# Optimization experiments

Measured on AMD Instinct MI355X. Metric: run time of the kernel, lower is better.

Reference implementation:

```python
import jax, jax.numpy as jnp
import numpy as np

N = 100000
E = 1600000
D_IN = 128
D_H = 128
D_OUT = 128
K = 2
EPS = 0.1


def setup_inputs() -> dict:
    key = jax.random.key(0)
    ks = jax.random.split(key, 10)
    x = jax.random.normal(ks[0], (N, D_IN), dtype=jnp.float32)
    edge_index = jax.random.randint(ks[1], (2, E), 0, N, dtype=jnp.int64)
    # parameters (scaled like torch default inits, small uniform)
    def lin(k, fan_in, shape):
        bound = 1.0 / np.sqrt(fan_in)
        return jax.random.uniform(k, shape, jnp.float32, -bound, bound)
    emb_w = lin(ks[2], D_IN, (D_IN, D_H))
    emb_b = lin(ks[3], D_IN, (D_H,))
    # TAGConv: K+1 linears (no bias) + one output bias
    conv_ws = jnp.stack([lin(ks[4 + i], D_H, (D_H, D_H)) for i in range(K + 1)])
    conv_b = lin(ks[7], D_H, (D_H,))
    ro_w = lin(ks[8], D_H, (D_H, D_OUT))
    ro_b = lin(ks[9], D_H, (D_OUT,))
    return {
        "x": x, "edge_index": edge_index, "delta_t": 4,
        "emb_w": emb_w, "emb_b": emb_b,
        "conv_ws": conv_ws, "conv_b": conv_b,
        "ro_w": ro_w, "ro_b": ro_b,
    }


def _tagconv(h, src, dst, norm, conv_ws, conv_b):
    """PyG TAGConv: out = sum_k W_k (A_hat^k h) + b, A_hat = D^-1/2 A D^-1/2 (no self loops)."""
    out = h @ conv_ws[0]
    xk = h
    for k in range(1, K + 1):
        msg = norm[:, None] * xk[src]            # [E, D_H] gather
        xk = jax.ops.segment_sum(msg, dst, num_segments=h.shape[0])  # scatter-add
        out = out + xk @ conv_ws[k]
    return out + conv_b


def reference(x, edge_index, delta_t, emb_w, emb_b, conv_ws, conv_b, ro_w, ro_b):
    src = edge_index[0]
    dst = edge_index[1]
    n = x.shape[0]
    # gcn_norm without self loops: deg over targets of unit edge weights
    deg = jnp.zeros((n,), jnp.float32).at[dst].add(1.0)
    dinv = jnp.where(deg > 0, jax.lax.rsqrt(jnp.maximum(deg, 1.0)), 0.0)
    norm = dinv[src] * dinv[dst]                 # [E]

    h = x @ emb_w + emb_b
    h_middle = h
    for _ in range(int(delta_t)):
        conv = _tagconv(h, src, dst, norm, conv_ws, conv_b)
        h_middle = h + 0.5 * EPS * jnp.tanh(conv)
        conv_mid = _tagconv(h_middle, src, dst, norm, conv_ws, conv_b)
        h = h + EPS * jnp.tanh(conv_mid)
    y = h_middle @ ro_w + ro_b
    return (y, h_middle)
```

## Files before the change

### kernel.cpp

```cpp
#include <hip/hip_runtime.h>
#include <hip/hip_bf16.h>

#define NN 100000
#define EE 1600000
#define DD 128
#define EPSc 0.1f

typedef unsigned short bfu;
typedef __attribute__((ext_vector_type(8))) short short8;
typedef __attribute__((ext_vector_type(4))) float f32x4;
typedef __attribute__((ext_vector_type(2))) float f32x2;

__device__ __forceinline__ float bf2f(bfu s) {
    union { unsigned u; float f; } c; c.u = ((unsigned)s) << 16; return c.f;
}
__device__ __forceinline__ bfu f2bf(float f) {
    union { float f; unsigned u; } c; c.f = f;
    unsigned u = c.u + 0x7fffu + ((c.u >> 16) & 1u);
    return (bfu)(u >> 16);
}
__device__ __forceinline__ unsigned pk8(float a, float b, float c, float d) {
    int r = 0;
    r = __builtin_amdgcn_cvt_pk_fp8_f32(a, b, r, false);
    r = __builtin_amdgcn_cvt_pk_fp8_f32(c, d, r, true);
    return (unsigned)r;
}
__device__ __forceinline__ unsigned char enc8(float a) {
    return (unsigned char)(__builtin_amdgcn_cvt_pk_fp8_f32(a, a, 0, false) & 0xFF);
}
__device__ __forceinline__ short8 e8bf(uint2 u) {
    f32x2 p0 = __builtin_amdgcn_cvt_pk_f32_fp8((int)u.x, false);
    f32x2 p1 = __builtin_amdgcn_cvt_pk_f32_fp8((int)u.x, true);
    f32x2 p2 = __builtin_amdgcn_cvt_pk_f32_fp8((int)u.y, false);
    f32x2 p3 = __builtin_amdgcn_cvt_pk_f32_fp8((int)u.y, true);
    short8 s;
    s[0] = (short)f2bf(p0[0]); s[1] = (short)f2bf(p0[1]);
    s[2] = (short)f2bf(p1[0]); s[3] = (short)f2bf(p1[1]);
    s[4] = (short)f2bf(p2[0]); s[5] = (short)f2bf(p2[1]);
    s[6] = (short)f2bf(p3[0]); s[7] = (short)f2bf(p3[1]);
    return s;
}


__global__ __launch_bounds__(256) void count_deg_kernel(const int* __restrict__ dst,
                                                        int* __restrict__ ideg, int e_cnt) {
    int e = blockIdx.x * 256 + threadIdx.x;
    if (e < e_cnt) atomicAdd(&ideg[dst[e]], 1);
}

__global__ __launch_bounds__(256) void dinv_kernel(const int* __restrict__ ideg,
                                                   float* __restrict__ dinv, int n) {
    int i = blockIdx.x * 256 + threadIdx.x;
    if (i < n) {
        int d = ideg[i];
        dinv[i] = (d > 0) ? rsqrtf((float)d) : 0.0f;
    }
}

__global__ __launch_bounds__(256) void partial_sum_kernel(const int* __restrict__ ideg,
                                                          int* __restrict__ partials, int n) {
    __shared__ int sm[256];
    int i = blockIdx.x * 256 + threadIdx.x;
    sm[threadIdx.x] = (i < n) ? ideg[i] : 0;
    __syncthreads();
    for (int off = 128; off > 0; off >>= 1) {
        if ((int)threadIdx.x < off) sm[threadIdx.x] += sm[threadIdx.x + off];
        __syncthreads();
    }
    if (threadIdx.x == 0) partials[blockIdx.x] = sm[0];
}

__global__ __launch_bounds__(512) void scan_partials_kernel(int* __restrict__ partials,
                                                            int* __restrict__ row_ptr,
                                                            int nb, int n) {
    __shared__ int sm[512];
    int v = ((int)threadIdx.x < nb) ? partials[threadIdx.x] : 0;
    sm[threadIdx.x] = v;
    __syncthreads();
    for (int off = 1; off < 512; off <<= 1) {
        int t = (threadIdx.x >= (unsigned)off) ? sm[threadIdx.x - off] : 0;
        __syncthreads();
        sm[threadIdx.x] += t;
        __syncthreads();
    }
    if ((int)threadIdx.x < nb) partials[threadIdx.x] = sm[threadIdx.x] - v;
    if (threadIdx.x == 511) row_ptr[n] = sm[511];
}

__global__ __launch_bounds__(256) void scan_block_kernel(const int* __restrict__ ideg,
                                                         const int* __restrict__ partials,
                                                         int* __restrict__ row_ptr,
                                                         int* __restrict__ cursor, int n) {
    __shared__ int sm[256];
    int i = blockIdx.x * 256 + threadIdx.x;
    int v = (i < n) ? ideg[i] : 0;
    sm[threadIdx.x] = v;
    __syncthreads();
    for (int off = 1; off < 256; off <<= 1) {
        int t = (threadIdx.x >= (unsigned)off) ? sm[threadIdx.x - off] : 0;
        __syncthreads();
        sm[threadIdx.x] += t;
        __syncthreads();
    }
    if (i < n) {
        int excl = partials[blockIdx.x] + sm[threadIdx.x] - v;
        row_ptr[i] = excl;
        cursor[i] = excl;
    }
}

__global__ __launch_bounds__(256) void fill_csr_kernel(const int* __restrict__ src,
                                                       const int* __restrict__ dst,
                                                       const float* __restrict__ dinv,
                                                       int* __restrict__ cursor,
                                                       unsigned* __restrict__ cvp, int e_cnt) {
    int e = blockIdx.x * 256 + threadIdx.x;
    if (e < e_cnt) {
        int d = dst[e], s = src[e];
        int pos = atomicAdd(&cursor[d], 1);
        unsigned vb = __float_as_uint(dinv[s] * dinv[d]);
        unsigned r = vb + 0xFFFFu + ((vb >> 17) & 1u);
        cvp[pos] = (r & 0xFFFE0000u) | (unsigned)s;
    }
}


__global__ __launch_bounds__(256) void wfrag_kernel(const float* __restrict__ conv_ws,
                                                    const float* __restrict__ ro_w,
                                                    bfu* __restrict__ Wf) {
    int m = blockIdx.x;
    const float* W = (m < 3) ? conv_ws + m * 16384 : ro_w;
    bfu* T = Wf + m * 16384;
    for (int j = 0; j < 64; ++j) {
        int i = threadIdx.x + j * 256;
        int k = i >> 7, n = i & 127;
        int nt = n >> 4, ks = k >> 5, kg = (k >> 3) & 3, jj = k & 7;
        int l = kg * 16 + (n & 15);
        int flat = ((nt * 4 + ks) * 64 + l) * 8 + jj;
        T[flat] = f2bf(W[i]);
    }
}


__device__ __forceinline__ void acc8f8(uint2 u, float v, float* acc) {
    f32x2 p0 = __builtin_amdgcn_cvt_pk_f32_fp8((int)u.x, false);
    f32x2 p1 = __builtin_amdgcn_cvt_pk_f32_fp8((int)u.x, true);
    f32x2 p2 = __builtin_amdgcn_cvt_pk_f32_fp8((int)u.y, false);
    f32x2 p3 = __builtin_amdgcn_cvt_pk_f32_fp8((int)u.y, true);
    acc[0] = fmaf(v, p0[0], acc[0]); acc[1] = fmaf(v, p0[1], acc[1]);
    acc[2] = fmaf(v, p1[0], acc[2]); acc[3] = fmaf(v, p1[1], acc[3]);
    acc[4] = fmaf(v, p2[0], acc[4]); acc[5] = fmaf(v, p2[1], acc[5]);
    acc[6] = fmaf(v, p3[0], acc[6]); acc[7] = fmaf(v, p3[1], acc[7]);
}

__global__ __launch_bounds__(256) void prop_kernel(const unsigned char* __restrict__ xin8,
                                                   unsigned char* __restrict__ out8,
                                                   const int* __restrict__ row_ptr,
                                                   const unsigned* __restrict__ cvp, int n) {
    int wid = (blockIdx.x * 256 + threadIdx.x) >> 6;
    int lane = threadIdx.x & 63;
    if (wid >= n) return;
    int s = row_ptr[wid];
    int deg = row_ptr[wid + 1] - s;
    int g = lane >> 4;
    int li = lane & 15;
    float acc[8] = {0.f, 0.f, 0.f, 0.f, 0.f, 0.f, 0.f, 0.f};
    for (int base = 0; base < deg; base += 64) {
        int cnt = deg - base; if (cnt > 64) cnt = 64;
        unsigned el = (lane < cnt) ? cvp[s + base + lane] : 0u;
        for (int q = 0; q < cnt; q += 16) {
            uint2 x[4]; float v[4];
            #pragma unroll
            for (int j = 0; j < 4; ++j) {
                int idx = q + j * 4 + g;
                unsigned c = __shfl(el, idx);
                bool valid = idx < cnt;
                v[j] = valid ? __uint_as_float(c & 0xFFFE0000u) : 0.f;
                x[j] = valid ? *(const uint2*)(xin8 + (size_t)(c & 0x1FFFFu) * DD + li * 8)
                             : make_uint2(0u, 0u);
            }
            #pragma unroll
            for (int j = 0; j < 4; ++j) acc8f8(x[j], v[j], acc);
        }
    }
    #pragma unroll
    for (int k = 0; k < 8; ++k) {
        acc[k] += __shfl_xor(acc[k], 16);
        acc[k] += __shfl_xor(acc[k], 32);
    }
    if (g == 0) {
        uint2 q;
        q.x = pk8(acc[0], acc[1], acc[2], acc[3]);
        q.y = pk8(acc[4], acc[5], acc[6], acc[7]);
        *(uint2*)(out8 + (size_t)wid * DD + li * 8) = q;
    }
}


template <int NMAT, bool TANH, bool A8>
__global__ __launch_bounds__(256) void mfma_mm_kernel(const void* __restrict__ A0,
                                                      const void* __restrict__ A1,
                                                      const void* __restrict__ A2,
                                                      const bfu* __restrict__ Wf,
                                                      const float* __restrict__ bias,
                                                      const bfu* __restrict__ base16,
                                                      float* __restrict__ outf,
                                                      bfu* __restrict__ out16,
                                                      unsigned char* __restrict__ out8,
                                                      float scale) {
    int tid = threadIdx.x;
    int wave = tid >> 6, lane = tid & 63;
    int r0 = blockIdx.x * 64 + wave * 16;
    int li = lane & 15, kg = lane >> 4;
    int rowA = r0 + li;
    bool rv = rowA < NN;
    size_t arow = (size_t)(rv ? rowA : 0) * DD;

    const void* As[3] = {A0, A1, A2};
    short8 a[NMAT][4];
    #pragma unroll
    for (int m = 0; m < NMAT; ++m) {
        #pragma unroll
        for (int ks = 0; ks < 4; ++ks) {
            short8 t;
            if (A8) {
                uint2 u = *(const uint2*)((const unsigned char*)As[m] + arow + ks * 32 + kg * 8);
                t = e8bf(u);
            } else {
                t = *(const short8*)((const bfu*)As[m] + arow + ks * 32 + kg * 8);
            }
            if (!rv) t = (short8)0;
            a[m][ks] = t;
        }
    }

    const short8* Bp = (const short8*)Wf;
    f32x4 acc[8];
    #pragma unroll
    for (int nt = 0; nt < 8; ++nt) acc[nt] = (f32x4)(0.f);
    #pragma unroll
    for (int nt = 0; nt < 8; ++nt) {
        #pragma unroll
        for (int m = 0; m < NMAT; ++m) {
            #pragma unroll
            for (int ks = 0; ks < 4; ++ks) {
                short8 b = Bp[m * 2048 + (nt * 4 + ks) * 64 + lane];
                acc[nt] = __builtin_amdgcn_mfma_f32_16x16x32_bf16(a[m][ks], b, acc[nt], 0, 0, 0);
            }
        }
    }

    #pragma unroll
    for (int nt = 0; nt < 8; ++nt) {
        int cc = nt * 16 + li;
        float bv = bias[cc];
        #pragma unroll
        for (int rg = 0; rg < 4; ++rg) {
            int rr = r0 + kg * 4 + rg;
            if (rr < NN) {
                size_t off = (size_t)rr * DD + cc;
                float o = acc[nt][rg];
                if (TANH) {
                    float ov = bf2f(base16[off]) + scale * tanhf(o + bv);
                    if (outf) outf[off] = ov;
                    if (out16) out16[off] = f2bf(ov);
                    out8[off] = enc8(ov);
                } else {
                    outf[off] = o + bv;
                }
            }
        }
    }
}


__global__ __launch_bounds__(256) void matmul_f32_kernel(const float* __restrict__ A,
                                                         const float* __restrict__ W,
                                                         const float* __restrict__ bias,
                                                         bfu* __restrict__ out16,
                                                         unsigned char* __restrict__ out8) {
    __shared__ float Wl[128][128];
    __shared__ float Al[32][128];
    int tid = threadIdx.x;

    const float4* Wv = (const float4*)W;
    float4* Wlv = (float4*)&Wl[0][0];
    #pragma unroll
    for (int i = 0; i < 16; ++i) Wlv[tid + i * 256] = Wv[tid + i * 256];

    size_t row0 = (size_t)blockIdx.x * 32;
    const float4* Av = (const float4*)(A + row0 * DD);
    float4* Alv = (float4*)&Al[0][0];
    #pragma unroll
    for (int i = 0; i < 4; ++i) Alv[tid + i * 256] = Av[tid + i * 256];
    __syncthreads();

    int cq = tid & 31;
    int rg = tid >> 5;
    float acc[4][4] = {};
    #pragma unroll 8
    for (int k = 0; k < 128; ++k) {
        float4 w = *(const float4*)&Wl[k][cq * 4];
        #pragma unroll
        for (int i = 0; i < 4; ++i) {
            float a = Al[rg * 4 + i][k];
            acc[i][0] = fmaf(a, w.x, acc[i][0]);
            acc[i][1] = fmaf(a, w.y, acc[i][1]);
            acc[i][2] = fmaf(a, w.z, acc[i][2]);
            acc[i][3] = fmaf(a, w.w, acc[i][3]);
        }
    }

    #pragma unroll
    for (int i = 0; i < 4; ++i) {
        size_t r = row0 + rg * 4 + i;
        float4 b = *(const float4*)(bias + cq * 4);
        float4 o = make_float4(acc[i][0] + b.x, acc[i][1] + b.y,
                               acc[i][2] + b.z, acc[i][3] + b.w);
        bfu q0 = f2bf(o.x), q1 = f2bf(o.y), q2 = f2bf(o.z), q3 = f2bf(o.w);
        *(uint2*)(out16 + r * DD + cq * 4) =
            make_uint2((unsigned)q0 | ((unsigned)q1 << 16), (unsigned)q2 | ((unsigned)q3 << 16));
        *(unsigned*)(out8 + r * DD + cq * 4) = pk8(o.x, o.y, o.z, o.w);
    }
}


extern "C" void kernel_launch(void* const* d_in, const int* in_sizes, int n_in,
                              void* d_out, int out_size, void* d_ws, size_t ws_size,
                              hipStream_t stream) {
    const float* x      = (const float*)d_in[0];
    const int*   eidx   = (const int*)d_in[1];
    const float* emb_w  = (const float*)d_in[3];
    const float* emb_b  = (const float*)d_in[4];
    const float* conv_ws = (const float*)d_in[5];
    const float* conv_b = (const float*)d_in[6];
    const float* ro_w   = (const float*)d_in[7];
    const float* ro_b   = (const float*)d_in[8];

    const int* src = eidx;
    const int* dst = eidx + EE;

    float* y  = (float*)d_out;
    float* hm = y + (size_t)NN * DD;

    char* p = (char*)d_ws;
    const size_t FB2 = (size_t)NN * DD * sizeof(bfu);
    const size_t FB1 = (size_t)NN * DD;
    bfu* h16     = (bfu*)p;                 p += FB2;
    bfu* hm16    = (bfu*)p;                 p += FB2;
    unsigned char* h8  = (unsigned char*)p; p += FB1;
    unsigned char* hm8 = (unsigned char*)p; p += FB1;
    unsigned char* bufA8 = (unsigned char*)p; p += FB1;
    unsigned char* bufB8 = (unsigned char*)p; p += FB1;
    float* dinv  = (float*)p;               p += (size_t)NN * 4;
    int* ideg    = (int*)p;                 p += (size_t)NN * 4;
    int* row_ptr = (int*)p;                 p += (size_t)(NN + 1) * 4;
    int* cursor  = (int*)p;                 p += (size_t)NN * 4;
    int* partials = (int*)p;                p += (size_t)512 * 4;
    bfu* Wf      = (bfu*)p;                 p += (size_t)4 * 16384 * sizeof(bfu);
    unsigned* cvp = (unsigned*)p;           p += (size_t)EE * 4;

    const int NB = (NN + 255) / 256;

    hipMemsetAsync(ideg, 0, (size_t)NN * 4, stream);
    count_deg_kernel<<<EE / 256, 256, 0, stream>>>(dst, ideg, EE);
    dinv_kernel<<<NB, 256, 0, stream>>>(ideg, dinv, NN);
    partial_sum_kernel<<<NB, 256, 0, stream>>>(ideg, partials, NN);
    scan_partials_kernel<<<1, 512, 0, stream>>>(partials, row_ptr, NB, NN);
    scan_block_kernel<<<NB, 256, 0, stream>>>(ideg, partials, row_ptr, cursor, NN);
    fill_csr_kernel<<<EE / 256, 256, 0, stream>>>(src, dst, dinv, cursor, cvp, EE);
    wfrag_kernel<<<4, 256, 0, stream>>>(conv_ws, ro_w, Wf);

    const int MM_GRID   = (NN + 63) / 64;
    const int PROP_GRID = NN * 64 / 256;

    matmul_f32_kernel<<<NN / 32, 256, 0, stream>>>(x, emb_w, emb_b, h16, h8);

    for (int t = 0; t < 4; ++t) {
        prop_kernel<<<PROP_GRID, 256, 0, stream>>>(h8, bufA8, row_ptr, cvp, NN);
        prop_kernel<<<PROP_GRID, 256, 0, stream>>>(bufA8, bufB8, row_ptr, cvp, NN);
        mfma_mm_kernel<3, true, true><<<MM_GRID, 256, 0, stream>>>(
            h8, bufA8, bufB8, Wf, conv_b, h16,
            (t == 3) ? hm : nullptr, (t == 3) ? hm16 : nullptr, hm8, 0.5f * EPSc);

        prop_kernel<<<PROP_GRID, 256, 0, stream>>>(hm8, bufA8, row_ptr, cvp, NN);
        prop_kernel<<<PROP_GRID, 256, 0, stream>>>(bufA8, bufB8, row_ptr, cvp, NN);
        mfma_mm_kernel<3, true, true><<<MM_GRID, 256, 0, stream>>>(
            hm8, bufA8, bufB8, Wf, conv_b, h16, nullptr, h16, h8, EPSc);
    }

    mfma_mm_kernel<1, false, false><<<MM_GRID, 256, 0, stream>>>(
        hm16, nullptr, nullptr, Wf + 3 * 16384, ro_b, nullptr, y, nullptr, nullptr, 0.f);
}
```

Baseline: 1.284 ms.

## Build CSR via dst-buckets and src-shard partial ordering per row

CSR construction now histograms edges per (dst, source-shard) pair, so each row's neighbors are grouped by source range. This should improve gather locality in the propagation kernels. Edges are first scattered into 256 destination buckets, and each bucket is then placed by one block, which localizes the atomic cursor traffic. The cost is extra preprocessing passes, a 16x larger counter array, and a fixed bucket capacity that silently drops edges if a bucket overflows.

```diff
diff --git a/kernel.cpp b/kernel.cpp
--- a/kernel.cpp
+++ b/kernel.cpp
@@ -5,6 +5,11 @@
 #define EE 1600000
 #define DD 128
 #define EPSc 0.1f
+#define NSH 16
+#define SHDIV 6250
+#define NBUK 256
+#define BDIV 391
+#define BCAP 7200
 
 typedef unsigned short bfu;
 typedef __attribute__((ext_vector_type(8))) short short8;
@@ -42,19 +47,30 @@
 }
 
 
-__global__ __launch_bounds__(256) void count_deg_kernel(const int* __restrict__ dst,
-                                                        int* __restrict__ ideg, int e_cnt) {
+__global__ __launch_bounds__(256) void hist_kernel(const int* __restrict__ src,
+                                                   const int* __restrict__ dst,
+                                                   int* __restrict__ cnt, int e_cnt) {
     int e = blockIdx.x * 256 + threadIdx.x;
-    if (e < e_cnt) atomicAdd(&ideg[dst[e]], 1);
-}
-
-__global__ __launch_bounds__(256) void dinv_kernel(const int* __restrict__ ideg,
-                                                   float* __restrict__ dinv, int n) {
+    if (e < e_cnt) {
+        int d = dst[e];
+        int sh = (unsigned)src[e] / SHDIV;
+        atomicAdd(&cnt[d * NSH + sh], 1);
+    }
+}
+
+__global__ __launch_bounds__(256) void offsets_kernel(int* __restrict__ cnt,
+                                                      int* __restrict__ ideg,
+                                                      float* __restrict__ dinv, int n) {
     int i = blockIdx.x * 256 + threadIdx.x;
-    if (i < n) {
-        int d = ideg[i];
-        dinv[i] = (d > 0) ? rsqrtf((float)d) : 0.0f;
-    }
+    if (i >= n) return;
+    int c[NSH];
+    #pragma unroll
+    for (int s = 0; s < NSH; ++s) c[s] = cnt[i * NSH + s];
+    int run = 0;
+    #pragma unroll
+    for (int s = 0; s < NSH; ++s) { int v = c[s]; cnt[i * NSH + s] = run; run += v; }
+    ideg[i] = run;
+    dinv[i] = (run > 0) ? rsqrtf((float)run) : 0.0f;
 }
 
 __global__ __launch_bounds__(256) void partial_sum_kernel(const int* __restrict__ ideg,
@@ -89,8 +105,9 @@
 
 __global__ __launch_bounds__(256) void scan_block_kernel(const int* __restrict__ ideg,
                                                          const int* __restrict__ partials,
+                                                         const int* __restrict__ prefix16,
                                                          int* __restrict__ row_ptr,
-                                                         int* __restrict__ cursor, int n) {
+                                                         int* __restrict__ cur16, int n) {
     __shared__ int sm[256];
     int i = blockIdx.x * 256 + threadIdx.x;
     int v = (i < n) ? ideg[i] : 0;
@@ -105,22 +122,43 @@
     if (i < n) {
         int excl = partials[blockIdx.x] + sm[threadIdx.x] - v;
         row_ptr[i] = excl;
-        cursor[i] = excl;
-    }
-}
-
-__global__ __launch_bounds__(256) void fill_csr_kernel(const int* __restrict__ src,
-                                                       const int* __restrict__ dst,
-                                                       const float* __restrict__ dinv,
-                                                       int* __restrict__ cursor,
-                                                       unsigned* __restrict__ cvp, int e_cnt) {
+        #pragma unroll
+        for (int s = 0; s < NSH; ++s) cur16[i * NSH + s] = excl + prefix16[i * NSH + s];
+    }
+}
+
+__global__ __launch_bounds__(256) void bucket_scatter_kernel(const int* __restrict__ src,
+                                                             const int* __restrict__ dst,
+                                                             const float* __restrict__ dinv,
+                                                             int* __restrict__ bcur,
+                                                             uint2* __restrict__ buckets,
+                                                             int e_cnt) {
     int e = blockIdx.x * 256 + threadIdx.x;
     if (e < e_cnt) {
         int d = dst[e], s = src[e];
-        int pos = atomicAdd(&cursor[d], 1);
-        unsigned vb = __float_as_uint(dinv[s] * dinv[d]);
-        unsigned r = vb + 0xFFFFu + ((vb >> 17) & 1u);
-        cvp[pos] = (r & 0xFFFE0000u) | (unsigned)s;
+        unsigned b = (unsigned)d / BDIV;
+        int pos = atomicAdd(&bcur[b], 1);
+        if (pos < BCAP) {
+            unsigned vb = __float_as_uint(dinv[s] * dinv[d]);
+            unsigned r = vb + 0xFFFFu + ((vb >> 17) & 1u);
+            buckets[(size_t)b * BCAP + pos] = make_uint2((r & 0xFFFE0000u) | (unsigned)s,
+                                                         (unsigned)d);
+        }
+    }
+}
+
+__global__ __launch_bounds__(256) void bucket_place_kernel(const uint2* __restrict__ buckets,
+                                                           const int* __restrict__ bcur,
+                                                           int* __restrict__ cur16,
+                                                           unsigned* __restrict__ cvp) {
+    int b = blockIdx.x;
+    int cnt = bcur[b]; if (cnt > BCAP) cnt = BCAP;
+    for (int i = threadIdx.x; i < cnt; i += 256) {
+        uint2 w = buckets[(size_t)b * BCAP + i];
+        unsigned col = w.x & 0x1FFFFu;
+        int sh = col / SHDIV;
+        int pos = atomicAdd(&cur16[w.y * NSH + sh], 1);
+        cvp[pos] = w.x;
     }
 }
 
@@ -355,20 +393,25 @@
     float* dinv  = (float*)p;               p += (size_t)NN * 4;
     int* ideg    = (int*)p;                 p += (size_t)NN * 4;
     int* row_ptr = (int*)p;                 p += (size_t)(NN + 1) * 4;
-    int* cursor  = (int*)p;                 p += (size_t)NN * 4;
     int* partials = (int*)p;                p += (size_t)512 * 4;
+    int* cnt     = (int*)p;                 p += (size_t)NN * NSH * 4;
+    int* cur16   = (int*)p;                 p += (size_t)NN * NSH * 4;
+    int* bcur    = (int*)p;                 p += (size_t)NBUK * 4;
+    uint2* buckets = (uint2*)p;             p += (size_t)NBUK * BCAP * 8;
     bfu* Wf      = (bfu*)p;                 p += (size_t)4 * 16384 * sizeof(bfu);
     unsigned* cvp = (unsigned*)p;           p += (size_t)EE * 4;
 
     const int NB = (NN + 255) / 256;
 
-    hipMemsetAsync(ideg, 0, (size_t)NN * 4, stream);
-    count_deg_kernel<<<EE / 256, 256, 0, stream>>>(dst, ideg, EE);
-    dinv_kernel<<<NB, 256, 0, stream>>>(ideg, dinv, NN);
+    hipMemsetAsync(cnt, 0, (size_t)NN * NSH * 4, stream);
+    hipMemsetAsync(bcur, 0, (size_t)NBUK * 4, stream);
+    hist_kernel<<<EE / 256, 256, 0, stream>>>(src, dst, cnt, EE);
+    offsets_kernel<<<NB, 256, 0, stream>>>(cnt, ideg, dinv, NN);
     partial_sum_kernel<<<NB, 256, 0, stream>>>(ideg, partials, NN);
     scan_partials_kernel<<<1, 512, 0, stream>>>(partials, row_ptr, NB, NN);
-    scan_block_kernel<<<NB, 256, 0, stream>>>(ideg, partials, row_ptr, cursor, NN);
-    fill_csr_kernel<<<EE / 256, 256, 0, stream>>>(src, dst, dinv, cursor, cvp, EE);
+    scan_block_kernel<<<NB, 256, 0, stream>>>(ideg, partials, cnt, row_ptr, cur16, NN);
+    bucket_scatter_kernel<<<EE / 256, 256, 0, stream>>>(src, dst, dinv, bcur, buckets, EE);
+    bucket_place_kernel<<<NBUK, 256, 0, stream>>>(buckets, bcur, cur16, cvp);
     wfrag_kernel<<<4, 256, 0, stream>>>(conv_ws, ro_w, Wf);
 
     const int MM_GRID   = (NN + 63) / 64;
```

New measurement: 2.027 ms. 1.58x slower.

## Skip unused final half-step and fuse readout matmul into last conv epilogue

Applied to the files above, without the earlier changes.

The final iteration's second half-step only updates h, which is never read after the loop. The launch schedule now skips its two propagations and one matmul. The readout matmul is fused into the epilogue of the last h_middle kernel: tiles go through LDS into a second MFMA pass, which removes the bf16 hm16 buffer and a separate launch. tanhf is also replaced with a clamped exp/rcp approximation, which adds small accuracy error and LDS use in the fused variant.

```diff
diff --git a/kernel.cpp b/kernel.cpp
--- a/kernel.cpp
+++ b/kernel.cpp
@@ -39,6 +39,11 @@
     s[4] = (short)f2bf(p2[0]); s[5] = (short)f2bf(p2[1]);
     s[6] = (short)f2bf(p3[0]); s[7] = (short)f2bf(p3[1]);
     return s;
+}
+__device__ __forceinline__ float ftanh(float x) {
+    float xc = fminf(fmaxf(x, -9.0f), 9.0f);
+    float e = __expf(2.0f * xc);
+    return (e - 1.0f) * __builtin_amdgcn_rcpf(e + 1.0f);
 }
 
 
@@ -197,7 +202,7 @@
 }
 
 
-template <int NMAT, bool TANH, bool A8>
+template <int NMAT, bool TANH, bool A8, bool RO>
 __global__ __launch_bounds__(256) void mfma_mm_kernel(const void* __restrict__ A0,
                                                       const void* __restrict__ A1,
                                                       const void* __restrict__ A2,
@@ -207,6 +212,9 @@
                                                       float* __restrict__ outf,
                                                       bfu* __restrict__ out16,
                                                       unsigned char* __restrict__ out8,
+                                                      const bfu* __restrict__ Wro,
+                                                      const float* __restrict__ rob,
+                                                      float* __restrict__ yout,
                                                       float scale) {
     int tid = threadIdx.x;
     int wave = tid >> 6, lane = tid & 63;
@@ -250,6 +258,9 @@
         }
     }
 
+    __shared__ bfu lds_a[RO ? 4 : 1][RO ? 2048 : 1];
+    bfu* myt = &lds_a[RO ? wave : 0][0];
+
     #pragma unroll
     for (int nt = 0; nt < 8; ++nt) {
         int cc = nt * 16 + li;
@@ -257,17 +268,47 @@
         #pragma unroll
         for (int rg = 0; rg < 4; ++rg) {
             int rr = r0 + kg * 4 + rg;
-            if (rr < NN) {
-                size_t off = (size_t)rr * DD + cc;
-                float o = acc[nt][rg];
-                if (TANH) {
-                    float ov = bf2f(base16[off]) + scale * tanhf(o + bv);
+            bool v = rr < NN;
+            size_t off = (size_t)(v ? rr : 0) * DD + cc;
+            float o = acc[nt][rg];
+            if (TANH) {
+                float ov = v ? (bf2f(base16[off]) + scale * ftanh(o + bv)) : 0.f;
+                if (v) {
                     if (outf) outf[off] = ov;
                     if (out16) out16[off] = f2bf(ov);
                     out8[off] = enc8(ov);
-                } else {
-                    outf[off] = o + bv;
                 }
+                if (RO) {
+                    int ks = nt >> 1;
+                    int kgk = ((nt & 1) << 1) | (li >> 3);
+                    int j = li & 7;
+                    int row = kg * 4 + rg;
+                    myt[(ks * 64 + kgk * 16 + row) * 8 + j] = f2bf(ov);
+                }
+            } else {
+                if (v) outf[off] = o + bv;
+            }
+        }
+    }
+
+    if (RO) {
+        short8 ar[4];
+        #pragma unroll
+        for (int ks = 0; ks < 4; ++ks)
+            ar[ks] = *(const short8*)&myt[(ks * 64 + lane) * 8];
+        const short8* Bro = (const short8*)Wro;
+        #pragma unroll
+        for (int nt = 0; nt < 8; ++nt) {
+            f32x4 ay = (f32x4)(0.f);
+            #pragma unroll
+            for (int ks = 0; ks < 4; ++ks)
+                ay = __builtin_amdgcn_mfma_f32_16x16x32_bf16(ar[ks], Bro[(nt * 4 + ks) * 64 + lane], ay, 0, 0, 0);
+            int cc = nt * 16 + li;
+            float bv = rob[cc];
+            #pragma unroll
+            for (int rg = 0; rg < 4; ++rg) {
+                int rr = r0 + kg * 4 + rg;
+                if (rr < NN) yout[(size_t)rr * DD + cc] = ay[rg] + bv;
             }
         }
     }
@@ -347,7 +388,6 @@
     const size_t FB2 = (size_t)NN * DD * sizeof(bfu);
     const size_t FB1 = (size_t)NN * DD;
     bfu* h16     = (bfu*)p;                 p += FB2;
-    bfu* hm16    = (bfu*)p;                 p += FB2;
     unsigned char* h8  = (unsigned char*)p; p += FB1;
     unsigned char* hm8 = (unsigned char*)p; p += FB1;
     unsigned char* bufA8 = (unsigned char*)p; p += FB1;
@@ -379,16 +419,20 @@
     for (int t = 0; t < 4; ++t) {
         prop_kernel<<<PROP_GRID, 256, 0, stream>>>(h8, bufA8, row_ptr, cvp, NN);
         prop_kernel<<<PROP_GRID, 256, 0, stream>>>(bufA8, bufB8, row_ptr, cvp, NN);
-        mfma_mm_kernel<3, true, true><<<MM_GRID, 256, 0, stream>>>(
-            h8, bufA8, bufB8, Wf, conv_b, h16,
-            (t == 3) ? hm : nullptr, (t == 3) ? hm16 : nullptr, hm8, 0.5f * EPSc);
-
-        prop_kernel<<<PROP_GRID, 256, 0, stream>>>(hm8, bufA8, row_ptr, cvp, NN);
-        prop_kernel<<<PROP_GRID, 256, 0, stream>>>(bufA8, bufB8, row_ptr, cvp, NN);
-        mfma_mm_kernel<3, true, true><<<MM_GRID, 256, 0, stream>>>(
-            hm8, bufA8, bufB8, Wf, conv_b, h16, nullptr, h16, h8, EPSc);
-    }
-
-    mfma_mm_kernel<1, false, false><<<MM_GRID, 256, 0, stream>>>(
-        hm16, nullptr, nullptr, Wf + 3 * 16384, ro_b, nullptr, y, nullptr, nullptr, 0.f);
-}
+        if (t < 3) {
+            mfma_mm_kernel<3, true, true, false><<<MM_GRID, 256, 0, stream>>>(
+                h8, bufA8, bufB8, Wf, conv_b, h16,
+                nullptr, nullptr, hm8, nullptr, nullptr, nullptr, 0.5f * EPSc);
+
+            prop_kernel<<<PROP_GRID, 256, 0, stream>>>(hm8, bufA8, row_ptr, cvp, NN);
+            prop_kernel<<<PROP_GRID, 256, 0, stream>>>(bufA8, bufB8, row_ptr, cvp, NN);
+            mfma_mm_kernel<3, true, true, false><<<MM_GRID, 256, 0, stream>>>(
+                hm8, bufA8, bufB8, Wf, conv_b, h16,
+                nullptr, h16, h8, nullptr, nullptr, nullptr, EPSc);
+        } else {
+            mfma_mm_kernel<3, true, true, true><<<MM_GRID, 256, 0, stream>>>(
+                h8, bufA8, bufB8, Wf, conv_b, h16,
+                hm, nullptr, hm8, Wf + 3 * 16384, ro_b, y, 0.5f * EPSc);
+        }
+    }
+}
```

Result: faster. 1.141 ms (-11.1%).
